# Performance work log

Hardware: AMD Instinct MI355X
Metric: run time of the kernel (lower is better)

Reference implementation:

```python
import jax, jax.numpy as jnp
import numpy as np

HEADS, DIM_HEAD, DIM = 8, 64, 512
INNER = HEADS * DIM_HEAD  # 512


def setup_inputs() -> dict:
    key = jax.random.key(0)
    k1, k2, k3 = jax.random.split(key, 3)
    b, n = 2, 2048
    x = jax.random.normal(k1, (b, n, DIM), dtype=jnp.float32)
    # to_qkv: Linear(dim, 4*inner_dim, bias=False); weight stored [out, in]
    w_qkv = jax.random.normal(k2, (4 * INNER, DIM), dtype=jnp.float32) * (1.0 / np.sqrt(DIM))
    # to_out: Linear(2*inner_dim, dim) with bias
    w_out = jax.random.normal(k3, (DIM, 2 * INNER), dtype=jnp.float32) * (1.0 / np.sqrt(2 * INNER))
    b_out = jnp.zeros((DIM,), dtype=jnp.float32)
    return {"x": x, "w_qkv": w_qkv, "w_out": w_out, "b_out": b_out}


def reference(x, w_qkv, w_out, b_out):
    b, n, d = x.shape
    qkvt = x @ w_qkv.T  # [b, n, 4*inner]
    q, k, v, t = jnp.split(qkvt, 4, axis=-1)

    def split_heads(z):
        return z.reshape(b, n, HEADS, DIM_HEAD).transpose(0, 2, 1, 3)  # [b,h,n,dh]

    q, k, v, t = map(split_heads, (q, k, v, t))

    scale = DIM_HEAD ** -0.5
    dots = jnp.einsum('bhid,bhjd->bhij', q, k) * scale
    attn1 = jax.nn.softmax(dots, axis=-1)

    # fixed positional-decay attention: exp(-|i-j|/e), torch broadcast-normalized
    idx = jnp.arange(1, n + 1, dtype=x.dtype)  # linspace(1, n, n)
    tg = jnp.abs(idx[None, :] - idx[:, None])  # [n, n]
    a2 = jnp.exp(-tg / jnp.exp(jnp.asarray(1.0, x.dtype)))
    a2 = a2 / a2.sum(-1)  # broadcasts over last axis, as in the torch code

    out1 = jnp.einsum('bhij,bhjd->bhid', attn1, v)
    out2 = jnp.einsum('ij,bhjd->bhid', a2, t)
    out = jnp.concatenate([out1, out2], axis=-1)  # [b,h,n,2*dh]
    out = out.transpose(0, 2, 1, 3).reshape(b, n, HEADS * 2 * DIM_HEAD)  # [b,n,2*inner]
    return out @ w_out.T + b_out
```

## Files before the change

kernel.cpp:

```cpp
#include <hip/hip_runtime.h>
#include <hip/hip_bf16.h>
#include <stdint.h>

typedef unsigned short u16;
typedef __bf16 bf16;
typedef __bf16 bf16x8 __attribute__((ext_vector_type(8)));
typedef float f32x4 __attribute__((ext_vector_type(4)));
typedef float f32x16 __attribute__((ext_vector_type(16)));

#define NSEQ 2048
#define NDH 64
#define NH 8
#define QKS 2097152ull

__device__ __forceinline__ float b2f(u16 u) {
  union { float f; uint32_t i; } x; x.i = ((uint32_t)u) << 16; return x.f;
}
__device__ __forceinline__ u16 f2b(float f) {
  union { float f; uint32_t i; } x; x.f = f;
  const uint32_t r = x.i + 0x7FFFu + ((x.i >> 16) & 1u);
  return (u16)(r >> 16);
}
__device__ __forceinline__ uint32_t b2pk(float a, float b) {
  union { __hip_bfloat162 h; uint32_t u; } x;
  x.h = __float22bfloat162_rn(make_float2(a, b));
  return x.u;
}
__device__ __forceinline__ void gl16(const void* g, void* l) {
  __builtin_amdgcn_global_load_lds(
      (const __attribute__((address_space(1))) void*)g,
      (__attribute__((address_space(3))) void*)l, 16, 0, 0);
}

__global__ __launch_bounds__(256) void k_cvt(
    const float* __restrict__ X, const float* __restrict__ Wq,
    const float* __restrict__ Wo, u16* __restrict__ Xb,
    u16* __restrict__ Wqb, u16* __restrict__ Wob) {
  const int b = blockIdx.x;
  const float* src; u16* dst; int idx;
  if (b < 1024)      { src = X;  dst = Xb;  idx = b; }
  else if (b < 1536) { src = Wq; dst = Wqb; idx = b - 1024; }
  else               { src = Wo; dst = Wob; idx = b - 1536; }
  const size_t off = ((size_t)idx * 256 + threadIdx.x) * 8;
  const float4 a = *(const float4*)(src + off);
  const float4 c = *(const float4*)(src + off + 4);
  uint4 o = {b2pk(a.x, a.y), b2pk(a.z, a.w), b2pk(c.x, c.y), b2pk(c.z, c.w)};
  *(uint4*)(dst + off) = o;
}

__global__ __launch_bounds__(256) void k_gemm_qkvt(
    const u16* __restrict__ Xb, const u16* __restrict__ Wb, u16* __restrict__ qkvt) {
  __shared__ __align__(16) bf16 smem[18432];
  bf16* A0e = smem;
  bf16* A1e = smem + 4096;
  bf16* B0e = smem + 8192;
  bf16* B1e = smem + 12288;
  const int tid = threadIdx.x;
  const int m0 = blockIdx.x * 128;
  const int n0 = blockIdx.y * 128;
  const int w = tid >> 6, lane = tid & 63;
  const int wy = w >> 1, wx = w & 1;
  const int quad = lane >> 4, l15 = lane & 15;
  const int srow = tid >> 2, sc8 = (tid & 3) * 8;
  const u16* ag = Xb + (size_t)(m0 + srow) * 512 + sc8;
  const u16* bg = Wb + (size_t)(n0 + srow) * 512 + sc8;
  char* aL00 = (char*)smem + w * 1024;
  char* aL01 = (char*)smem + 4096  + w * 1024;
  char* aL10 = (char*)smem + 8192  + w * 1024;
  char* aL11 = (char*)smem + 12288 + w * 1024;
  char* bL00 = (char*)smem + 16384 + w * 1024;
  char* bL01 = (char*)smem + 20480 + w * 1024;
  char* bL10 = (char*)smem + 24576 + w * 1024;
  char* bL11 = (char*)smem + 28672 + w * 1024;
  f32x4 acc[4][4];
#pragma unroll
  for (int mt = 0; mt < 4; ++mt)
#pragma unroll
    for (int nt = 0; nt < 4; ++nt) acc[mt][nt] = (f32x4){0.f, 0.f, 0.f, 0.f};
  for (int kc = 0; kc < 512; kc += 64) {
    __syncthreads();
    gl16(ag + kc,                 aL00);
    gl16(ag + kc + 64 * 512,      aL01);
    gl16(ag + kc + 32,            aL10);
    gl16(ag + kc + 32 + 64 * 512, aL11);
    gl16(bg + kc,                 bL00);
    gl16(bg + kc + 64 * 512,      bL01);
    gl16(bg + kc + 32,            bL10);
    gl16(bg + kc + 32 + 64 * 512, bL11);
    __syncthreads();
#pragma unroll
    for (int ks = 0; ks < 2; ++ks) {
      const bf16* Ae = ks ? A1e : A0e;
      const bf16* Be = ks ? B1e : B0e;
      bf16x8 afr[4], bfr[4];
#pragma unroll
      for (int mt = 0; mt < 4; ++mt)
        afr[mt] = *(const bf16x8*)&Ae[(wy * 64 + mt * 16 + l15) * 32 + quad * 8];
#pragma unroll
      for (int nt = 0; nt < 4; ++nt)
        bfr[nt] = *(const bf16x8*)&Be[(wx * 64 + nt * 16 + l15) * 32 + quad * 8];
#pragma unroll
      for (int mt = 0; mt < 4; ++mt)
#pragma unroll
        for (int nt = 0; nt < 4; ++nt)
          acc[mt][nt] = __builtin_amdgcn_mfma_f32_16x16x32_bf16(afr[mt], bfr[nt], acc[mt][nt], 0, 0, 0);
    }
  }
  __syncthreads();
  const int cbase = n0 + wx * 64;
  const int which = cbase >> 9;
  const int h     = (cbase >> 6) & 7;
  const float scale = (which == 0) ? 0.18033688011112043f : 1.0f;
  bf16* Cw = smem + w * 4608;
  if (which == 2) {
#pragma unroll
    for (int nt = 0; nt < 4; ++nt)
#pragma unroll
      for (int mt = 0; mt < 4; ++mt)
#pragma unroll
        for (int r = 0; r < 4; ++r)
          Cw[(nt * 16 + l15) * 72 + mt * 16 + quad * 4 + r] = (bf16)acc[mt][nt][r];
  } else {
#pragma unroll
    for (int mt = 0; mt < 4; ++mt)
#pragma unroll
      for (int nt = 0; nt < 4; ++nt)
#pragma unroll
        for (int r = 0; r < 4; ++r)
          Cw[(mt * 16 + quad * 4 + r) * 72 + nt * 16 + l15] = (bf16)(acc[mt][nt][r] * scale);
  }
  const int mb = m0 + wy * 64;
  const int bb = mb >> 11;
  const int nn0 = mb & (NSEQ - 1);
  if (which == 2) {
    u16* vt = qkvt + 2ull * QKS + (size_t)(bb * NH + h) * NDH * NSEQ;
#pragma unroll
    for (int p = 0; p < 8; ++p) {
      const int d = p * 8 + (lane >> 3);
      const int t8 = (lane & 7) * 8;
      const uint4 v = *(const uint4*)&Cw[d * 72 + t8];
      *(uint4*)(vt + (size_t)d * NSEQ + nn0 + t8) = v;
    }
  } else {
    u16* dst = qkvt + (size_t)which * QKS + ((size_t)(bb * NH + h) * NSEQ + nn0) * NDH;
#pragma unroll
    for (int p = 0; p < 8; ++p) {
      const int tok = p * 8 + (lane >> 3);
      const int c8 = (lane & 7) * 8;
      const uint4 v = *(const uint4*)&Cw[tok * 72 + c8];
      *(uint4*)(dst + (size_t)tok * NDH + c8) = v;
    }
  }
}

__global__ __launch_bounds__(256) void k_attn_band(
    const u16* __restrict__ qkvt, u16* __restrict__ out12) {
  __shared__ __align__(16) char usmem[72704];
  const int tid = threadIdx.x;
  const int bid = blockIdx.x;
  if (bid < 512) {
    bf16* Qs = (bf16*)usmem;
    bf16* KV = Qs + 4608;
    bf16* Pw = KV + 9216;
    float* Lpart = (float*)(usmem + 46080);
    bf16* Ks = KV;
    bf16* Vt = KV + 64 * 72;
    const int bh  = bid & 15;
    const int q0  = (bid >> 4) * 64;
    const size_t base  = (size_t)bh * (NSEQ * NDH);
    const size_t vbase = 2ull * QKS + (size_t)bh * (NDH * NSEQ);
    const int wq = tid >> 6, lane = tid & 63;
    const int qh = wq >> 1, kh = wq & 1;
    const int l31 = lane & 31, hi = lane >> 5;
    const int srow = tid >> 2, sc0 = (tid & 3) * 16;
    {
      const u16* qp = qkvt + base + (size_t)(q0 + srow) * NDH + sc0;
      *(uint4*)&Qs[srow * 72 + sc0]     = *(const uint4*)qp;
      *(uint4*)&Qs[srow * 72 + sc0 + 8] = *(const uint4*)(qp + 8);
    }
    __syncthreads();
    bf16x8 qb[4];
#pragma unroll
    for (int c = 0; c < 4; ++c)
      qb[c] = *(const bf16x8*)&Qs[(qh * 32 + l31) * 72 + c * 16 + hi * 8];
    float lacc = 0.f;
    f32x16 o[2];
#pragma unroll
    for (int nt = 0; nt < 2; ++nt)
#pragma unroll
      for (int r = 0; r < 16; ++r) o[nt][r] = 0.f;
    const u16* kp = qkvt + QKS + base + (size_t)srow * NDH + sc0;
    const u16* vp = qkvt + vbase + (size_t)srow * NSEQ + sc0;
    uint4 k0 = *(const uint4*)kp;
    uint4 k1 = *(const uint4*)(kp + 8);
    uint4 v0 = *(const uint4*)vp;
    uint4 v1 = *(const uint4*)(vp + 8);
    for (int kt = 0; kt < 32; ++kt) {
      __syncthreads();
      *(uint4*)&Ks[srow * 72 + sc0]     = k0;
      *(uint4*)&Ks[srow * 72 + sc0 + 8] = k1;
      *(uint4*)&Vt[srow * 72 + sc0]     = v0;
      *(uint4*)&Vt[srow * 72 + sc0 + 8] = v1;
      __syncthreads();
      if (kt < 31) {
        const u16* kn = kp + (size_t)(kt + 1) * 64 * NDH;
        const u16* vn = vp + (kt + 1) * 64;
        k0 = *(const uint4*)kn;
        k1 = *(const uint4*)(kn + 8);
        v0 = *(const uint4*)vn;
        v1 = *(const uint4*)(vn + 8);
      }
      f32x16 s;
#pragma unroll
      for (int r = 0; r < 16; ++r) s[r] = 0.f;
      __builtin_amdgcn_s_setprio(1);
#pragma unroll
      for (int c = 0; c < 4; ++c) {
        const bf16x8 ka = *(const bf16x8*)&Ks[(kh * 32 + l31) * 72 + c * 16 + hi * 8];
        s = __builtin_amdgcn_mfma_f32_32x32x16_bf16(ka, qb[c], s, 0, 0, 0);
      }
      __builtin_amdgcn_s_setprio(0);
      float ts = 0.f;
#pragma unroll
      for (int r = 0; r < 16; ++r) {
        s[r] = __builtin_amdgcn_exp2f(s[r]);
        ts += s[r];
      }
      ts += __shfl_xor(ts, 32);
      lacc += ts;
      bf16* pr = Pw + (wq * 32 + l31) * 72;
#pragma unroll
      for (int g = 0; g < 4; ++g) {
        uint2 t = {b2pk(s[4 * g], s[4 * g + 1]), b2pk(s[4 * g + 2], s[4 * g + 3])};
        *(uint2*)&pr[g * 8 + hi * 4] = t;
      }
      __builtin_amdgcn_s_setprio(1);
#pragma unroll
      for (int c = 0; c < 2; ++c) {
        const bf16x8 pa = *(const bf16x8*)&Pw[(wq * 32 + l31) * 72 + c * 16 + hi * 8];
        const bf16x8 vb0 = *(const bf16x8*)&Vt[l31 * 72 + kh * 32 + c * 16 + hi * 8];
        const bf16x8 vb1 = *(const bf16x8*)&Vt[(32 + l31) * 72 + kh * 32 + c * 16 + hi * 8];
        o[0] = __builtin_amdgcn_mfma_f32_32x32x16_bf16(pa, vb0, o[0], 0, 0, 0);
        o[1] = __builtin_amdgcn_mfma_f32_32x32x16_bf16(pa, vb1, o[1], 0, 0, 0);
      }
      __builtin_amdgcn_s_setprio(0);
    }
    __syncthreads();
    if (lane < 32) Lpart[wq * 32 + lane] = lacc;
    float* Osum = (float*)KV;
    if (kh == 1) {
#pragma unroll
      for (int nt = 0; nt < 2; ++nt)
#pragma unroll
        for (int r = 0; r < 16; ++r) {
          const int row = (r & 3) + 8 * (r >> 2) + 4 * hi;
          Osum[(qh * 32 + row) * 64 + nt * 32 + l31] = o[nt][r];
        }
    }
    __syncthreads();
    if (kh == 0) {
      const int bb = bh >> 3, h = bh & 7;
#pragma unroll
      for (int r = 0; r < 16; ++r) {
        const int row = (r & 3) + 8 * (r >> 2) + 4 * hi;
        const float lt = Lpart[qh * 2 * 32 + row] + Lpart[(qh * 2 + 1) * 32 + row];
        const float inv = 1.f / lt;
        const int nn = q0 + qh * 32 + row;
        u16* dst = out12 + (size_t)(bb * NSEQ + nn) * 1024 + h * 128;
        dst[l31]      = f2b((o[0][r] + Osum[(qh * 32 + row) * 64 + l31]) * inv);
        dst[32 + l31] = f2b((o[1][r] + Osum[(qh * 32 + row) * 64 + 32 + l31]) * inv);
      }
    }
  } else {
    float* sinv = (float*)usmem;
    float* fb   = (float*)(usmem + 3072);
    const int cb = bid - 512;
    const int w = tid >> 6, d = tid & 63;
    const int c  = (cb & 7) * 4 + w;
    const int i0 = c * 64;
    const int bh = cb >> 3;
    const size_t tb = 3ull * QKS + (size_t)bh * (NSEQ * NDH);
    const float EI = 0.36787944117144233f;
    const float RR = 0.69220062755534635f;
    const float OMR = 1.f - RR;
#pragma unroll
    for (int p = 0; p < 3; ++p) {
      const int j = i0 - 64 + p * 64 + d;
      const float r1 = __expf(-(float)(j + 1) * EI);
      const float r2 = __expf(-(float)(NSEQ - j) * EI);
      sinv[w * 192 + p * 64 + d] = OMR / (1.f - r1 + RR - r2);
    }
    const u16* tp = qkvt + tb + d;
    float f = 0.f;
    if (c > 0) {
#pragma unroll 8
      for (int jj = 0; jj < 64; ++jj)
        f = RR * f + sinv[w * 192 + jj] * b2f(tp[(size_t)(i0 - 64 + jj) * NDH]);
    }
#pragma unroll 8
    for (int jj = 0; jj < 64; ++jj) {
      f = RR * f + sinv[w * 192 + 64 + jj] * b2f(tp[(size_t)(i0 + jj) * NDH]);
      fb[(w * 64 + jj) * 68 + d] = f;
    }
    float b = 0.f;
    if (c < 31) {
#pragma unroll 8
      for (int jj = 63; jj >= 0; --jj)
        b = RR * b + sinv[w * 192 + 128 + jj] * b2f(tp[(size_t)(i0 + 64 + jj) * NDH]);
    }
    const int bb = bh >> 3, h = bh & 7;
#pragma unroll 8
    for (int jj = 63; jj >= 0; --jj) {
      const float g = sinv[w * 192 + 64 + jj] * b2f(tp[(size_t)(i0 + jj) * NDH]);
      b = RR * b + g;
      out12[(size_t)(bb * NSEQ + i0 + jj) * 1024 + h * 128 + 64 + d] =
          f2b(fb[(w * 64 + jj) * 68 + d] + b - g);
    }
  }
}

__global__ __launch_bounds__(256) void k_gemm_out(
    const u16* __restrict__ A, const u16* __restrict__ Wb,
    const float* __restrict__ bias, float* __restrict__ out) {
  __shared__ __align__(16) float smemf[6144];
  bf16* A0e = (bf16*)smemf;
  bf16* A1e = (bf16*)smemf + 4096;
  bf16* B0e = (bf16*)smemf + 8192;
  bf16* B1e = (bf16*)smemf + 10240;
  const int tid = threadIdx.x;
  const int m0 = blockIdx.x * 128;
  const int n0 = blockIdx.y * 64;
  const int w = tid >> 6, lane = tid & 63;
  const int wy = w >> 1, wx = w & 1;
  const int quad = lane >> 4, l15 = lane & 15;
  const int srow = tid >> 2, sc8 = (tid & 3) * 8;
  const u16* ap = A  + (size_t)(m0 + srow) * 1024 + sc8;
  const u16* bp = Wb + (size_t)(n0 + srow) * 1024 + sc8;
  char* aL00 = (char*)smemf + w * 1024;
  char* aL01 = (char*)smemf + 4096  + w * 1024;
  char* aL10 = (char*)smemf + 8192  + w * 1024;
  char* aL11 = (char*)smemf + 12288 + w * 1024;
  char* bL0  = (char*)smemf + 16384 + w * 1024;
  char* bL1  = (char*)smemf + 20480 + w * 1024;
  f32x4 acc[4][2];
#pragma unroll
  for (int mt = 0; mt < 4; ++mt)
#pragma unroll
    for (int nt = 0; nt < 2; ++nt) acc[mt][nt] = (f32x4){0.f, 0.f, 0.f, 0.f};
  for (int kc = 0; kc < 1024; kc += 64) {
    __syncthreads();
    gl16(ap + kc,                  aL00);
    gl16(ap + kc + 64 * 1024,      aL01);
    gl16(ap + kc + 32,             aL10);
    gl16(ap + kc + 32 + 64 * 1024, aL11);
    gl16(bp + kc,                  bL0);
    gl16(bp + kc + 32,             bL1);
    __syncthreads();
#pragma unroll
    for (int ks = 0; ks < 2; ++ks) {
      const bf16* Ae = ks ? A1e : A0e;
      const bf16* Be = ks ? B1e : B0e;
      bf16x8 afr[4], bfr[2];
#pragma unroll
      for (int mt = 0; mt < 4; ++mt)
        afr[mt] = *(const bf16x8*)&Ae[(wy * 64 + mt * 16 + l15) * 32 + quad * 8];
#pragma unroll
      for (int nt = 0; nt < 2; ++nt)
        bfr[nt] = *(const bf16x8*)&Be[(wx * 32 + nt * 16 + l15) * 32 + quad * 8];
#pragma unroll
      for (int mt = 0; mt < 4; ++mt)
#pragma unroll
        for (int nt = 0; nt < 2; ++nt)
          acc[mt][nt] = __builtin_amdgcn_mfma_f32_16x16x32_bf16(afr[mt], bfr[nt], acc[mt][nt], 0, 0, 0);
    }
  }
  float bias_v[2];
#pragma unroll
  for (int nt = 0; nt < 2; ++nt) bias_v[nt] = bias[n0 + wx * 32 + nt * 16 + l15];
  __syncthreads();
  float* Cw = smemf + w * 576;
  const int erow = lane >> 2, ec8 = (lane & 3) * 8;
#pragma unroll
  for (int mt = 0; mt < 4; ++mt) {
#pragma unroll
    for (int nt = 0; nt < 2; ++nt)
#pragma unroll
      for (int r = 0; r < 4; ++r)
        Cw[(quad * 4 + r) * 36 + nt * 16 + l15] = acc[mt][nt][r] + bias_v[nt];
    const float4 v0 = *(const float4*)&Cw[erow * 36 + ec8];
    const float4 v1 = *(const float4*)&Cw[erow * 36 + ec8 + 4];
    float* op = out + (size_t)(m0 + wy * 64 + mt * 16 + erow) * 512 + n0 + wx * 32 + ec8;
    *(float4*)op       = v0;
    *(float4*)(op + 4) = v1;
  }
}

extern "C" void kernel_launch(void* const* d_in, const int* in_sizes, int n_in,
                              void* d_out, int out_size, void* d_ws, size_t ws_size,
                              hipStream_t stream) {
  (void)in_sizes; (void)n_in; (void)out_size; (void)ws_size;
  const float* x     = (const float*)d_in[0];
  const float* w_qkv = (const float*)d_in[1];
  const float* w_out = (const float*)d_in[2];
  const float* b_out = (const float*)d_in[3];
  float* out = (float*)d_out;
  u16* ws    = (u16*)d_ws;
  u16* qkvt  = ws;
  u16* out12 = ws + 8ull  * 1024 * 1024;
  u16* Xb    = ws + 12ull * 1024 * 1024;
  u16* Wqb   = ws + 14ull * 1024 * 1024;
  u16* Wob   = ws + 15ull * 1024 * 1024;
  k_cvt      <<<dim3(1792), 256, 0, stream>>>(x, w_qkv, w_out, Xb, Wqb, Wob);
  k_gemm_qkvt<<<dim3(32, 16), 256, 0, stream>>>(Xb, Wqb, qkvt);
  k_attn_band<<<dim3(640), 256, 0, stream>>>(qkvt, out12);
  k_gemm_out <<<dim3(32, 8), 256, 0, stream>>>(out12, Wob, b_out, out);
}
```

Baseline: 141.3 us.

## Split attention and band kernels; load K/V fragments directly from global per wave

After: 176.3 us. 24.8% more time.

```diff
diff --git a/kernel.cpp b/kernel.cpp
--- a/kernel.cpp
+++ b/kernel.cpp
@@ -153,169 +153,149 @@
   }
 }
 
-__global__ __launch_bounds__(256) void k_attn_band(
+__global__ __launch_bounds__(256) void k_attn(
     const u16* __restrict__ qkvt, u16* __restrict__ out12) {
-  __shared__ __align__(16) char usmem[72704];
+  __shared__ float Os[4][32][64];
+  __shared__ float Lp[4][32];
   const int tid = threadIdx.x;
   const int bid = blockIdx.x;
-  if (bid < 512) {
-    bf16* Qs = (bf16*)usmem;
-    bf16* KV = Qs + 4608;
-    bf16* Pw = KV + 9216;
-    float* Lpart = (float*)(usmem + 46080);
-    bf16* Ks = KV;
-    bf16* Vt = KV + 64 * 72;
-    const int bh  = bid & 15;
-    const int q0  = (bid >> 4) * 64;
-    const size_t base  = (size_t)bh * (NSEQ * NDH);
-    const size_t vbase = 2ull * QKS + (size_t)bh * (NDH * NSEQ);
-    const int wq = tid >> 6, lane = tid & 63;
-    const int qh = wq >> 1, kh = wq & 1;
-    const int l31 = lane & 31, hi = lane >> 5;
-    const int srow = tid >> 2, sc0 = (tid & 3) * 16;
-    {
-      const u16* qp = qkvt + base + (size_t)(q0 + srow) * NDH + sc0;
-      *(uint4*)&Qs[srow * 72 + sc0]     = *(const uint4*)qp;
-      *(uint4*)&Qs[srow * 72 + sc0 + 8] = *(const uint4*)(qp + 8);
-    }
-    __syncthreads();
-    bf16x8 qb[4];
+  const int bh = bid & 15;
+  const int qt = bid >> 4;
+  const size_t base  = (size_t)bh * (NSEQ * NDH);
+  const size_t vbase = 2ull * QKS + (size_t)bh * (NDH * NSEQ);
+  const int wq = tid >> 6, lane = tid & 63;
+  const int l31 = lane & 31, hi = lane >> 5;
+  const u16* qp = qkvt + base + (size_t)(qt * 32 + l31) * NDH + hi * 8;
+  bf16x8 qb[4];
+#pragma unroll
+  for (int c = 0; c < 4; ++c) qb[c] = *(const bf16x8*)(qp + c * 16);
+  const u16* kp = qkvt + QKS + base + (size_t)(wq * 512 + l31) * NDH + hi * 8;
+  const u16* vp = qkvt + vbase + (size_t)wq * 512 + hi * 8;
+  float lacc = 0.f;
+  f32x16 o[2];
+#pragma unroll
+  for (int nt = 0; nt < 2; ++nt)
+#pragma unroll
+    for (int r = 0; r < 16; ++r) o[nt][r] = 0.f;
+  bf16x8 kf[4];
+#pragma unroll
+  for (int c = 0; c < 4; ++c) kf[c] = *(const bf16x8*)(kp + c * 16);
+  for (int t = 0; t < 16; ++t) {
+    bf16x8 vf[2][2];
+#pragma unroll
+    for (int nt = 0; nt < 2; ++nt)
+#pragma unroll
+      for (int c = 0; c < 2; ++c)
+        vf[nt][c] = *(const bf16x8*)(vp + (size_t)(nt * 32 + l31) * NSEQ + t * 32 + c * 16);
+    f32x16 s;
+#pragma unroll
+    for (int r = 0; r < 16; ++r) s[r] = 0.f;
+    __builtin_amdgcn_s_setprio(1);
 #pragma unroll
     for (int c = 0; c < 4; ++c)
-      qb[c] = *(const bf16x8*)&Qs[(qh * 32 + l31) * 72 + c * 16 + hi * 8];
-    float lacc = 0.f;
-    f32x16 o[2];
-#pragma unroll
-    for (int nt = 0; nt < 2; ++nt)
-#pragma unroll
-      for (int r = 0; r < 16; ++r) o[nt][r] = 0.f;
-    const u16* kp = qkvt + QKS + base + (size_t)srow * NDH + sc0;
-    const u16* vp = qkvt + vbase + (size_t)srow * NSEQ + sc0;
-    uint4 k0 = *(const uint4*)kp;
-    uint4 k1 = *(const uint4*)(kp + 8);
-    uint4 v0 = *(const uint4*)vp;
-    uint4 v1 = *(const uint4*)(vp + 8);
-    for (int kt = 0; kt < 32; ++kt) {
-      __syncthreads();
-      *(uint4*)&Ks[srow * 72 + sc0]     = k0;
-      *(uint4*)&Ks[srow * 72 + sc0 + 8] = k1;
-      *(uint4*)&Vt[srow * 72 + sc0]     = v0;
-      *(uint4*)&Vt[srow * 72 + sc0 + 8] = v1;
-      __syncthreads();
-      if (kt < 31) {
-        const u16* kn = kp + (size_t)(kt + 1) * 64 * NDH;
-        const u16* vn = vp + (kt + 1) * 64;
-        k0 = *(const uint4*)kn;
-        k1 = *(const uint4*)(kn + 8);
-        v0 = *(const uint4*)vn;
-        v1 = *(const uint4*)(vn + 8);
-      }
-      f32x16 s;
-#pragma unroll
-      for (int r = 0; r < 16; ++r) s[r] = 0.f;
-      __builtin_amdgcn_s_setprio(1);
-#pragma unroll
-      for (int c = 0; c < 4; ++c) {
-        const bf16x8 ka = *(const bf16x8*)&Ks[(kh * 32 + l31) * 72 + c * 16 + hi * 8];
-        s = __builtin_amdgcn_mfma_f32_32x32x16_bf16(ka, qb[c], s, 0, 0, 0);
-      }
-      __builtin_amdgcn_s_setprio(0);
-      float ts = 0.f;
-#pragma unroll
-      for (int r = 0; r < 16; ++r) {
-        s[r] = __builtin_amdgcn_exp2f(s[r]);
-        ts += s[r];
-      }
-      ts += __shfl_xor(ts, 32);
-      lacc += ts;
-      bf16* pr = Pw + (wq * 32 + l31) * 72;
-#pragma unroll
-      for (int g = 0; g < 4; ++g) {
-        uint2 t = {b2pk(s[4 * g], s[4 * g + 1]), b2pk(s[4 * g + 2], s[4 * g + 3])};
-        *(uint2*)&pr[g * 8 + hi * 4] = t;
-      }
-      __builtin_amdgcn_s_setprio(1);
-#pragma unroll
-      for (int c = 0; c < 2; ++c) {
-        const bf16x8 pa = *(const bf16x8*)&Pw[(wq * 32 + l31) * 72 + c * 16 + hi * 8];
-        const bf16x8 vb0 = *(const bf16x8*)&Vt[l31 * 72 + kh * 32 + c * 16 + hi * 8];
-        const bf16x8 vb1 = *(const bf16x8*)&Vt[(32 + l31) * 72 + kh * 32 + c * 16 + hi * 8];
-        o[0] = __builtin_amdgcn_mfma_f32_32x32x16_bf16(pa, vb0, o[0], 0, 0, 0);
-        o[1] = __builtin_amdgcn_mfma_f32_32x32x16_bf16(pa, vb1, o[1], 0, 0, 0);
-      }
-      __builtin_amdgcn_s_setprio(0);
-    }
-    __syncthreads();
-    if (lane < 32) Lpart[wq * 32 + lane] = lacc;
-    float* Osum = (float*)KV;
-    if (kh == 1) {
-#pragma unroll
-      for (int nt = 0; nt < 2; ++nt)
-#pragma unroll
-        for (int r = 0; r < 16; ++r) {
-          const int row = (r & 3) + 8 * (r >> 2) + 4 * hi;
-          Osum[(qh * 32 + row) * 64 + nt * 32 + l31] = o[nt][r];
-        }
-    }
-    __syncthreads();
-    if (kh == 0) {
-      const int bb = bh >> 3, h = bh & 7;
-#pragma unroll
-      for (int r = 0; r < 16; ++r) {
-        const int row = (r & 3) + 8 * (r >> 2) + 4 * hi;
-        const float lt = Lpart[qh * 2 * 32 + row] + Lpart[(qh * 2 + 1) * 32 + row];
-        const float inv = 1.f / lt;
-        const int nn = q0 + qh * 32 + row;
-        u16* dst = out12 + (size_t)(bb * NSEQ + nn) * 1024 + h * 128;
-        dst[l31]      = f2b((o[0][r] + Osum[(qh * 32 + row) * 64 + l31]) * inv);
-        dst[32 + l31] = f2b((o[1][r] + Osum[(qh * 32 + row) * 64 + 32 + l31]) * inv);
-      }
-    }
-  } else {
-    float* sinv = (float*)usmem;
-    float* fb   = (float*)(usmem + 3072);
-    const int cb = bid - 512;
-    const int w = tid >> 6, d = tid & 63;
-    const int c  = (cb & 7) * 4 + w;
-    const int i0 = c * 64;
-    const int bh = cb >> 3;
-    const size_t tb = 3ull * QKS + (size_t)bh * (NSEQ * NDH);
-    const float EI = 0.36787944117144233f;
-    const float RR = 0.69220062755534635f;
-    const float OMR = 1.f - RR;
-#pragma unroll
-    for (int p = 0; p < 3; ++p) {
-      const int j = i0 - 64 + p * 64 + d;
-      const float r1 = __expf(-(float)(j + 1) * EI);
-      const float r2 = __expf(-(float)(NSEQ - j) * EI);
-      sinv[w * 192 + p * 64 + d] = OMR / (1.f - r1 + RR - r2);
-    }
-    const u16* tp = qkvt + tb + d;
-    float f = 0.f;
-    if (c > 0) {
+      s = __builtin_amdgcn_mfma_f32_32x32x16_bf16(kf[c], qb[c], s, 0, 0, 0);
+    __builtin_amdgcn_s_setprio(0);
+    const int tn = (t + 1) & 15;
+    bf16x8 kfn[4];
+#pragma unroll
+    for (int c = 0; c < 4; ++c)
+      kfn[c] = *(const bf16x8*)(kp + (size_t)tn * 32 * NDH + c * 16);
+    float ts = 0.f;
+#pragma unroll
+    for (int r = 0; r < 16; ++r) {
+      s[r] = __builtin_amdgcn_exp2f(s[r]);
+      ts += s[r];
+    }
+    ts += __shfl_xor(ts, 32);
+    lacc += ts;
+    const uint32_t w0 = b2pk(s[0], s[1]),   w1 = b2pk(s[2], s[3]);
+    const uint32_t w2 = b2pk(s[4], s[5]),   w3 = b2pk(s[6], s[7]);
+    const uint32_t w4 = b2pk(s[8], s[9]),   w5 = b2pk(s[10], s[11]);
+    const uint32_t w6 = b2pk(s[12], s[13]), w7 = b2pk(s[14], s[15]);
+    const uint32_t e0 = __shfl_xor(hi ? w0 : w2, 32);
+    const uint32_t e1 = __shfl_xor(hi ? w1 : w3, 32);
+    const uint32_t e2 = __shfl_xor(hi ? w4 : w6, 32);
+    const uint32_t e3 = __shfl_xor(hi ? w5 : w7, 32);
+    uint4 u0 = hi ? (uint4){e0, e1, w2, w3} : (uint4){w0, w1, e0, e1};
+    uint4 u1 = hi ? (uint4){e2, e3, w6, w7} : (uint4){w4, w5, e2, e3};
+    const bf16x8 pa0 = *(const bf16x8*)&u0;
+    const bf16x8 pa1 = *(const bf16x8*)&u1;
+    __builtin_amdgcn_s_setprio(1);
+    o[0] = __builtin_amdgcn_mfma_f32_32x32x16_bf16(pa0, vf[0][0], o[0], 0, 0, 0);
+    o[0] = __builtin_amdgcn_mfma_f32_32x32x16_bf16(pa1, vf[0][1], o[0], 0, 0, 0);
+    o[1] = __builtin_amdgcn_mfma_f32_32x32x16_bf16(pa0, vf[1][0], o[1], 0, 0, 0);
+    o[1] = __builtin_amdgcn_mfma_f32_32x32x16_bf16(pa1, vf[1][1], o[1], 0, 0, 0);
+    __builtin_amdgcn_s_setprio(0);
+#pragma unroll
+    for (int c = 0; c < 4; ++c) kf[c] = kfn[c];
+  }
+#pragma unroll
+  for (int nt = 0; nt < 2; ++nt)
+#pragma unroll
+    for (int r = 0; r < 16; ++r) {
+      const int row = (r & 3) + 8 * (r >> 2) + 4 * hi;
+      Os[wq][row][nt * 32 + l31] = o[nt][r];
+    }
+  if (lane < 32) Lp[wq][lane] = lacc;
+  __syncthreads();
+  const int bb = bh >> 3, h = bh & 7;
+#pragma unroll
+  for (int rr = 0; rr < 8; ++rr) {
+    const int row = wq * 8 + rr;
+    const float lt = Lp[0][row] + Lp[1][row] + Lp[2][row] + Lp[3][row];
+    const float inv = 1.f / lt;
+    const float sum = Os[0][row][lane] + Os[1][row][lane] +
+                      Os[2][row][lane] + Os[3][row][lane];
+    out12[(size_t)(bb * NSEQ + qt * 32 + row) * 1024 + h * 128 + lane] =
+        f2b(sum * inv);
+  }
+}
+
+__global__ __launch_bounds__(256) void k_band(
+    const u16* __restrict__ qkvt, u16* __restrict__ out12) {
+  __shared__ float sinv[4][192];
+  __shared__ float fbuf[4][64][68];
+  const int tid = threadIdx.x;
+  const int w = tid >> 6, d = tid & 63;
+  const int c  = blockIdx.x * 4 + w;
+  const int i0 = c * 64;
+  const int bh = blockIdx.y;
+  const size_t tb = 3ull * QKS + (size_t)bh * (NSEQ * NDH);
+  const float EI = 0.36787944117144233f;
+  const float RR = 0.69220062755534635f;
+  const float OMR = 1.f - RR;
+#pragma unroll
+  for (int p = 0; p < 3; ++p) {
+    const int j = i0 - 64 + p * 64 + d;
+    const float r1 = __expf(-(float)(j + 1) * EI);
+    const float r2 = __expf(-(float)(NSEQ - j) * EI);
+    sinv[w][p * 64 + d] = OMR / (1.f - r1 + RR - r2);
+  }
+  const u16* tp = qkvt + tb + d;
+  float f = 0.f;
+  if (c > 0) {
 #pragma unroll 8
-      for (int jj = 0; jj < 64; ++jj)
-        f = RR * f + sinv[w * 192 + jj] * b2f(tp[(size_t)(i0 - 64 + jj) * NDH]);
-    }
+    for (int jj = 0; jj < 64; ++jj)
+      f = RR * f + sinv[w][jj] * b2f(tp[(size_t)(i0 - 64 + jj) * NDH]);
+  }
 #pragma unroll 8
-    for (int jj = 0; jj < 64; ++jj) {
-      f = RR * f + sinv[w * 192 + 64 + jj] * b2f(tp[(size_t)(i0 + jj) * NDH]);
-      fb[(w * 64 + jj) * 68 + d] = f;
-    }
-    float b = 0.f;
-    if (c < 31) {
+  for (int jj = 0; jj < 64; ++jj) {
+    f = RR * f + sinv[w][64 + jj] * b2f(tp[(size_t)(i0 + jj) * NDH]);
+    fbuf[w][jj][d] = f;
+  }
+  float b = 0.f;
+  if (c < 31) {
 #pragma unroll 8
-      for (int jj = 63; jj >= 0; --jj)
-        b = RR * b + sinv[w * 192 + 128 + jj] * b2f(tp[(size_t)(i0 + 64 + jj) * NDH]);
-    }
-    const int bb = bh >> 3, h = bh & 7;
+    for (int jj = 63; jj >= 0; --jj)
+      b = RR * b + sinv[w][128 + jj] * b2f(tp[(size_t)(i0 + 64 + jj) * NDH]);
+  }
+  const int bb = bh >> 3, h = bh & 7;
 #pragma unroll 8
-    for (int jj = 63; jj >= 0; --jj) {
-      const float g = sinv[w * 192 + 64 + jj] * b2f(tp[(size_t)(i0 + jj) * NDH]);
-      b = RR * b + g;
-      out12[(size_t)(bb * NSEQ + i0 + jj) * 1024 + h * 128 + 64 + d] =
-          f2b(fb[(w * 64 + jj) * 68 + d] + b - g);
-    }
+  for (int jj = 63; jj >= 0; --jj) {
+    const float g = sinv[w][64 + jj] * b2f(tp[(size_t)(i0 + jj) * NDH]);
+    b = RR * b + g;
+    out12[(size_t)(bb * NSEQ + i0 + jj) * 1024 + h * 128 + 64 + d] =
+        f2b(fbuf[w][jj][d] + b - g);
   }
 }
 
@@ -412,6 +392,7 @@
   u16* Wob   = ws + 15ull * 1024 * 1024;
   k_cvt      <<<dim3(1792), 256, 0, stream>>>(x, w_qkv, w_out, Xb, Wqb, Wob);
   k_gemm_qkvt<<<dim3(32, 16), 256, 0, stream>>>(Xb, Wqb, qkvt);
-  k_attn_band<<<dim3(640), 256, 0, stream>>>(qkvt, out12);
+  k_attn     <<<dim3(1024), 256, 0, stream>>>(qkvt, out12);
+  k_band     <<<dim3(8, 16), 256, 0, stream>>>(qkvt, out12);
   k_gemm_out <<<dim3(32, 8), 256, 0, stream>>>(out12, Wob, b_out, out);
 }
```

## Split fused attention/band kernel and pass P through registers via lane shuffles

Applied to the files above, without the earlier changes.

Measured after the change: 149.3 us. +5.7%, slower.

```diff
diff --git a/kernel.cpp b/kernel.cpp
--- a/kernel.cpp
+++ b/kernel.cpp
@@ -153,169 +153,175 @@
   }
 }
 
-__global__ __launch_bounds__(256) void k_attn_band(
+__global__ __launch_bounds__(256) void k_attn(
     const u16* __restrict__ qkvt, u16* __restrict__ out12) {
-  __shared__ __align__(16) char usmem[72704];
+  __shared__ __align__(16) bf16 Qs[64 * 72];
+  __shared__ __align__(16) bf16 KV[2 * 64 * 72];
+  __shared__ float Lpart[4][32];
+  bf16* Ks = KV;
+  bf16* Vt = KV + 64 * 72;
   const int tid = threadIdx.x;
-  const int bid = blockIdx.x;
-  if (bid < 512) {
-    bf16* Qs = (bf16*)usmem;
-    bf16* KV = Qs + 4608;
-    bf16* Pw = KV + 9216;
-    float* Lpart = (float*)(usmem + 46080);
-    bf16* Ks = KV;
-    bf16* Vt = KV + 64 * 72;
-    const int bh  = bid & 15;
-    const int q0  = (bid >> 4) * 64;
-    const size_t base  = (size_t)bh * (NSEQ * NDH);
-    const size_t vbase = 2ull * QKS + (size_t)bh * (NDH * NSEQ);
-    const int wq = tid >> 6, lane = tid & 63;
-    const int qh = wq >> 1, kh = wq & 1;
-    const int l31 = lane & 31, hi = lane >> 5;
-    const int srow = tid >> 2, sc0 = (tid & 3) * 16;
+  const int bh  = blockIdx.x;
+  const int q0  = blockIdx.y * 64;
+  const size_t base  = (size_t)bh * (NSEQ * NDH);
+  const size_t vbase = 2ull * QKS + (size_t)bh * (NDH * NSEQ);
+  const int wq = tid >> 6, lane = tid & 63;
+  const int qh = wq >> 1, kh = wq & 1;
+  const int l31 = lane & 31, hi = lane >> 5;
+  const int srow = tid >> 2, sc0 = (tid & 3) * 16;
+  {
+    const u16* qp = qkvt + base + (size_t)(q0 + srow) * NDH + sc0;
+    *(uint4*)&Qs[srow * 72 + sc0]     = *(const uint4*)qp;
+    *(uint4*)&Qs[srow * 72 + sc0 + 8] = *(const uint4*)(qp + 8);
+  }
+  __syncthreads();
+  bf16x8 qb[4];
+#pragma unroll
+  for (int c = 0; c < 4; ++c)
+    qb[c] = *(const bf16x8*)&Qs[(qh * 32 + l31) * 72 + c * 16 + hi * 8];
+  float lacc = 0.f;
+  f32x16 o[2];
+#pragma unroll
+  for (int nt = 0; nt < 2; ++nt)
+#pragma unroll
+    for (int r = 0; r < 16; ++r) o[nt][r] = 0.f;
+  const u16* kp = qkvt + QKS + base + (size_t)srow * NDH + sc0;
+  const u16* vp = qkvt + vbase + (size_t)srow * NSEQ + sc0;
+  uint4 k0 = *(const uint4*)kp;
+  uint4 k1 = *(const uint4*)(kp + 8);
+  uint4 v0 = *(const uint4*)vp;
+  uint4 v1 = *(const uint4*)(vp + 8);
+  for (int kt = 0; kt < 32; ++kt) {
+    __syncthreads();
+    *(uint4*)&Ks[srow * 72 + sc0]     = k0;
+    *(uint4*)&Ks[srow * 72 + sc0 + 8] = k1;
+    *(uint4*)&Vt[srow * 72 + sc0]     = v0;
+    *(uint4*)&Vt[srow * 72 + sc0 + 8] = v1;
+    __syncthreads();
+    if (kt < 31) {
+      const u16* kn = kp + (size_t)(kt + 1) * 64 * NDH;
+      const u16* vn = vp + (kt + 1) * 64;
+      k0 = *(const uint4*)kn;
+      k1 = *(const uint4*)(kn + 8);
+      v0 = *(const uint4*)vn;
+      v1 = *(const uint4*)(vn + 8);
+    }
+    f32x16 s;
+#pragma unroll
+    for (int r = 0; r < 16; ++r) s[r] = 0.f;
+    __builtin_amdgcn_s_setprio(1);
+#pragma unroll
+    for (int c = 0; c < 4; ++c) {
+      const bf16x8 ka = *(const bf16x8*)&Ks[(kh * 32 + l31) * 72 + c * 16 + hi * 8];
+      s = __builtin_amdgcn_mfma_f32_32x32x16_bf16(ka, qb[c], s, 0, 0, 0);
+    }
+    __builtin_amdgcn_s_setprio(0);
+    float ts = 0.f;
+#pragma unroll
+    for (int r = 0; r < 16; ++r) {
+      s[r] = __builtin_amdgcn_exp2f(s[r]);
+      ts += s[r];
+    }
+    ts += __shfl_xor(ts, 32);
+    lacc += ts;
+    const uint32_t w0 = b2pk(s[0], s[1]),   w1 = b2pk(s[2], s[3]);
+    const uint32_t w2 = b2pk(s[4], s[5]),   w3 = b2pk(s[6], s[7]);
+    const uint32_t w4 = b2pk(s[8], s[9]),   w5 = b2pk(s[10], s[11]);
+    const uint32_t w6 = b2pk(s[12], s[13]), w7 = b2pk(s[14], s[15]);
+    const uint32_t e0 = __shfl_xor(hi ? w0 : w2, 32);
+    const uint32_t e1 = __shfl_xor(hi ? w1 : w3, 32);
+    const uint32_t e2 = __shfl_xor(hi ? w4 : w6, 32);
+    const uint32_t e3 = __shfl_xor(hi ? w5 : w7, 32);
+    uint4 u0 = hi ? (uint4){e0, e1, w2, w3} : (uint4){w0, w1, e0, e1};
+    uint4 u1 = hi ? (uint4){e2, e3, w6, w7} : (uint4){w4, w5, e2, e3};
+    const bf16x8 pa0 = *(const bf16x8*)&u0;
+    const bf16x8 pa1 = *(const bf16x8*)&u1;
+    __builtin_amdgcn_s_setprio(1);
     {
-      const u16* qp = qkvt + base + (size_t)(q0 + srow) * NDH + sc0;
-      *(uint4*)&Qs[srow * 72 + sc0]     = *(const uint4*)qp;
-      *(uint4*)&Qs[srow * 72 + sc0 + 8] = *(const uint4*)(qp + 8);
-    }
-    __syncthreads();
-    bf16x8 qb[4];
-#pragma unroll
-    for (int c = 0; c < 4; ++c)
-      qb[c] = *(const bf16x8*)&Qs[(qh * 32 + l31) * 72 + c * 16 + hi * 8];
-    float lacc = 0.f;
-    f32x16 o[2];
+      const bf16x8 vb00 = *(const bf16x8*)&Vt[l31 * 72        + kh * 32 + hi * 8];
+      const bf16x8 vb10 = *(const bf16x8*)&Vt[(32 + l31) * 72 + kh * 32 + hi * 8];
+      o[0] = __builtin_amdgcn_mfma_f32_32x32x16_bf16(pa0, vb00, o[0], 0, 0, 0);
+      o[1] = __builtin_amdgcn_mfma_f32_32x32x16_bf16(pa0, vb10, o[1], 0, 0, 0);
+      const bf16x8 vb01 = *(const bf16x8*)&Vt[l31 * 72        + kh * 32 + 16 + hi * 8];
+      const bf16x8 vb11 = *(const bf16x8*)&Vt[(32 + l31) * 72 + kh * 32 + 16 + hi * 8];
+      o[0] = __builtin_amdgcn_mfma_f32_32x32x16_bf16(pa1, vb01, o[0], 0, 0, 0);
+      o[1] = __builtin_amdgcn_mfma_f32_32x32x16_bf16(pa1, vb11, o[1], 0, 0, 0);
+    }
+    __builtin_amdgcn_s_setprio(0);
+  }
+  __syncthreads();
+  if (lane < 32) Lpart[wq][lane] = lacc;
+  float* Osum = (float*)KV;
+  if (kh == 1) {
 #pragma unroll
     for (int nt = 0; nt < 2; ++nt)
-#pragma unroll
-      for (int r = 0; r < 16; ++r) o[nt][r] = 0.f;
-    const u16* kp = qkvt + QKS + base + (size_t)srow * NDH + sc0;
-    const u16* vp = qkvt + vbase + (size_t)srow * NSEQ + sc0;
-    uint4 k0 = *(const uint4*)kp;
-    uint4 k1 = *(const uint4*)(kp + 8);
-    uint4 v0 = *(const uint4*)vp;
-    uint4 v1 = *(const uint4*)(vp + 8);
-    for (int kt = 0; kt < 32; ++kt) {
-      __syncthreads();
-      *(uint4*)&Ks[srow * 72 + sc0]     = k0;
-      *(uint4*)&Ks[srow * 72 + sc0 + 8] = k1;
-      *(uint4*)&Vt[srow * 72 + sc0]     = v0;
-      *(uint4*)&Vt[srow * 72 + sc0 + 8] = v1;
-      __syncthreads();
-      if (kt < 31) {
-        const u16* kn = kp + (size_t)(kt + 1) * 64 * NDH;
-        const u16* vn = vp + (kt + 1) * 64;
-        k0 = *(const uint4*)kn;
-        k1 = *(const uint4*)(kn + 8);
-        v0 = *(const uint4*)vn;
-        v1 = *(const uint4*)(vn + 8);
-      }
-      f32x16 s;
-#pragma unroll
-      for (int r = 0; r < 16; ++r) s[r] = 0.f;
-      __builtin_amdgcn_s_setprio(1);
-#pragma unroll
-      for (int c = 0; c < 4; ++c) {
-        const bf16x8 ka = *(const bf16x8*)&Ks[(kh * 32 + l31) * 72 + c * 16 + hi * 8];
-        s = __builtin_amdgcn_mfma_f32_32x32x16_bf16(ka, qb[c], s, 0, 0, 0);
-      }
-      __builtin_amdgcn_s_setprio(0);
-      float ts = 0.f;
-#pragma unroll
-      for (int r = 0; r < 16; ++r) {
-        s[r] = __builtin_amdgcn_exp2f(s[r]);
-        ts += s[r];
-      }
-      ts += __shfl_xor(ts, 32);
-      lacc += ts;
-      bf16* pr = Pw + (wq * 32 + l31) * 72;
-#pragma unroll
-      for (int g = 0; g < 4; ++g) {
-        uint2 t = {b2pk(s[4 * g], s[4 * g + 1]), b2pk(s[4 * g + 2], s[4 * g + 3])};
-        *(uint2*)&pr[g * 8 + hi * 4] = t;
-      }
-      __builtin_amdgcn_s_setprio(1);
-#pragma unroll
-      for (int c = 0; c < 2; ++c) {
-        const bf16x8 pa = *(const bf16x8*)&Pw[(wq * 32 + l31) * 72 + c * 16 + hi * 8];
-        const bf16x8 vb0 = *(const bf16x8*)&Vt[l31 * 72 + kh * 32 + c * 16 + hi * 8];
-        const bf16x8 vb1 = *(const bf16x8*)&Vt[(32 + l31) * 72 + kh * 32 + c * 16 + hi * 8];
-        o[0] = __builtin_amdgcn_mfma_f32_32x32x16_bf16(pa, vb0, o[0], 0, 0, 0);
-        o[1] = __builtin_amdgcn_mfma_f32_32x32x16_bf16(pa, vb1, o[1], 0, 0, 0);
-      }
-      __builtin_amdgcn_s_setprio(0);
-    }
-    __syncthreads();
-    if (lane < 32) Lpart[wq * 32 + lane] = lacc;
-    float* Osum = (float*)KV;
-    if (kh == 1) {
-#pragma unroll
-      for (int nt = 0; nt < 2; ++nt)
-#pragma unroll
-        for (int r = 0; r < 16; ++r) {
-          const int row = (r & 3) + 8 * (r >> 2) + 4 * hi;
-          Osum[(qh * 32 + row) * 64 + nt * 32 + l31] = o[nt][r];
-        }
-    }
-    __syncthreads();
-    if (kh == 0) {
-      const int bb = bh >> 3, h = bh & 7;
 #pragma unroll
       for (int r = 0; r < 16; ++r) {
         const int row = (r & 3) + 8 * (r >> 2) + 4 * hi;
-        const float lt = Lpart[qh * 2 * 32 + row] + Lpart[(qh * 2 + 1) * 32 + row];
-        const float inv = 1.f / lt;
-        const int nn = q0 + qh * 32 + row;
-        u16* dst = out12 + (size_t)(bb * NSEQ + nn) * 1024 + h * 128;
-        dst[l31]      = f2b((o[0][r] + Osum[(qh * 32 + row) * 64 + l31]) * inv);
-        dst[32 + l31] = f2b((o[1][r] + Osum[(qh * 32 + row) * 64 + 32 + l31]) * inv);
+        Osum[(qh * 32 + row) * 64 + nt * 32 + l31] = o[nt][r];
       }
-    }
-  } else {
-    float* sinv = (float*)usmem;
-    float* fb   = (float*)(usmem + 3072);
-    const int cb = bid - 512;
-    const int w = tid >> 6, d = tid & 63;
-    const int c  = (cb & 7) * 4 + w;
-    const int i0 = c * 64;
-    const int bh = cb >> 3;
-    const size_t tb = 3ull * QKS + (size_t)bh * (NSEQ * NDH);
-    const float EI = 0.36787944117144233f;
-    const float RR = 0.69220062755534635f;
-    const float OMR = 1.f - RR;
-#pragma unroll
-    for (int p = 0; p < 3; ++p) {
-      const int j = i0 - 64 + p * 64 + d;
-      const float r1 = __expf(-(float)(j + 1) * EI);
-      const float r2 = __expf(-(float)(NSEQ - j) * EI);
-      sinv[w * 192 + p * 64 + d] = OMR / (1.f - r1 + RR - r2);
-    }
-    const u16* tp = qkvt + tb + d;
-    float f = 0.f;
-    if (c > 0) {
+  }
+  __syncthreads();
+  if (kh == 0) {
+    const int bb = bh >> 3, h = bh & 7;
+#pragma unroll
+    for (int r = 0; r < 16; ++r) {
+      const int row = (r & 3) + 8 * (r >> 2) + 4 * hi;
+      const float lt = Lpart[qh * 2][row] + Lpart[qh * 2 + 1][row];
+      const float inv = 1.f / lt;
+      const int nn = q0 + qh * 32 + row;
+      u16* dst = out12 + (size_t)(bb * NSEQ + nn) * 1024 + h * 128;
+      dst[l31]      = f2b((o[0][r] + Osum[(qh * 32 + row) * 64 + l31]) * inv);
+      dst[32 + l31] = f2b((o[1][r] + Osum[(qh * 32 + row) * 64 + 32 + l31]) * inv);
+    }
+  }
+}
+
+__global__ __launch_bounds__(256) void k_band(
+    const u16* __restrict__ qkvt, u16* __restrict__ out12) {
+  __shared__ float sinv[4][192];
+  __shared__ float fbuf[4][64][68];
+  const int tid = threadIdx.x;
+  const int w = tid >> 6, d = tid & 63;
+  const int c  = blockIdx.x * 4 + w;
+  const int i0 = c * 64;
+  const int bh = blockIdx.y;
+  const size_t tb = 3ull * QKS + (size_t)bh * (NSEQ * NDH);
+  const float EI = 0.36787944117144233f;
+  const float RR = 0.69220062755534635f;
+  const float OMR = 1.f - RR;
+#pragma unroll
+  for (int p = 0; p < 3; ++p) {
+    const int j = i0 - 64 + p * 64 + d;
+    const float r1 = __expf(-(float)(j + 1) * EI);
+    const float r2 = __expf(-(float)(NSEQ - j) * EI);
+    sinv[w][p * 64 + d] = OMR / (1.f - r1 + RR - r2);
+  }
+  const u16* tp = qkvt + tb + d;
+  float f = 0.f;
+  if (c > 0) {
 #pragma unroll 8
-      for (int jj = 0; jj < 64; ++jj)
-        f = RR * f + sinv[w * 192 + jj] * b2f(tp[(size_t)(i0 - 64 + jj) * NDH]);
-    }
+    for (int jj = 0; jj < 64; ++jj)
+      f = RR * f + sinv[w][jj] * b2f(tp[(size_t)(i0 - 64 + jj) * NDH]);
+  }
 #pragma unroll 8
-    for (int jj = 0; jj < 64; ++jj) {
-      f = RR * f + sinv[w * 192 + 64 + jj] * b2f(tp[(size_t)(i0 + jj) * NDH]);
-      fb[(w * 64 + jj) * 68 + d] = f;
-    }
-    float b = 0.f;
-    if (c < 31) {
+  for (int jj = 0; jj < 64; ++jj) {
+    f = RR * f + sinv[w][64 + jj] * b2f(tp[(size_t)(i0 + jj) * NDH]);
+    fbuf[w][jj][d] = f;
+  }
+  float b = 0.f;
+  if (c < 31) {
 #pragma unroll 8
-      for (int jj = 63; jj >= 0; --jj)
-        b = RR * b + sinv[w * 192 + 128 + jj] * b2f(tp[(size_t)(i0 + 64 + jj) * NDH]);
-    }
-    const int bb = bh >> 3, h = bh & 7;
+    for (int jj = 63; jj >= 0; --jj)
+      b = RR * b + sinv[w][128 + jj] * b2f(tp[(size_t)(i0 + 64 + jj) * NDH]);
+  }
+  const int bb = bh >> 3, h = bh & 7;
 #pragma unroll 8
-    for (int jj = 63; jj >= 0; --jj) {
-      const float g = sinv[w * 192 + 64 + jj] * b2f(tp[(size_t)(i0 + jj) * NDH]);
-      b = RR * b + g;
-      out12[(size_t)(bb * NSEQ + i0 + jj) * 1024 + h * 128 + 64 + d] =
-          f2b(fb[(w * 64 + jj) * 68 + d] + b - g);
-    }
+  for (int jj = 63; jj >= 0; --jj) {
+    const float g = sinv[w][64 + jj] * b2f(tp[(size_t)(i0 + jj) * NDH]);
+    b = RR * b + g;
+    out12[(size_t)(bb * NSEQ + i0 + jj) * 1024 + h * 128 + 64 + d] =
+        f2b(fbuf[w][jj][d] + b - g);
   }
 }
 
@@ -412,6 +418,7 @@
   u16* Wob   = ws + 15ull * 1024 * 1024;
   k_cvt      <<<dim3(1792), 256, 0, stream>>>(x, w_qkv, w_out, Xb, Wqb, Wob);
   k_gemm_qkvt<<<dim3(32, 16), 256, 0, stream>>>(Xb, Wqb, qkvt);
-  k_attn_band<<<dim3(640), 256, 0, stream>>>(qkvt, out12);
+  k_attn     <<<dim3(16, 32), 256, 0, stream>>>(qkvt, out12);
+  k_band     <<<dim3(8, 16), 256, 0, stream>>>(qkvt, out12);
   k_gemm_out <<<dim3(32, 8), 256, 0, stream>>>(out12, Wob, b_out, out);
 }
```
